# Kernel tuning notes

Measured on AMD Instinct MI355X. Metric: run time of the kernel, lower is better.

The kernel has to match this reference:

```python
import math
import jax, jax.numpy as jnp
import numpy as np

EMBED_DIM = 2048
NUM_HEADS = 16
HEAD_DIM = EMBED_DIM // NUM_HEADS
CHUNK = 128
RMS_EPS = 1e-5


def _build_slopes(n):
    # ALiBi-style slopes (power-of-2 branch; n=16 is a power of 2)
    def pow2(n):
        start = 2.0 ** (-(2.0 ** -(math.log2(n) - 3)))
        return [start * (start ** i) for i in range(n)]
    if math.log2(n).is_integer():
        s = pow2(n)
    else:
        closest = 2 ** math.floor(math.log2(n))
        s = pow2(closest) + pow2(2 * closest)[0::2][: n - closest]
    return jnp.asarray(s, dtype=jnp.float32)


def _rotary(x_BTHD, offset=0):
    # x: [B, T, H, D]; D//4 nonzero freqs + D//4 zero freqs -> D//2 angles
    T, D = x_BTHD.shape[1], x_BTHD.shape[-1]
    freq = (1.0 / 1024.0) ** jnp.linspace(0.0, 1.0, D // 4, dtype=jnp.float32)
    freq = jnp.concatenate([freq, jnp.zeros(D // 4, dtype=jnp.float32)])
    t = jnp.arange(offset, offset + T, dtype=jnp.float32)
    theta = t[:, None] * freq[None, :]            # [T, D/2]
    cos = jnp.cos(theta)[None, :, None, :]
    sin = jnp.sin(theta)[None, :, None, :]
    x1, x2 = jnp.split(x_BTHD.astype(jnp.float32), 2, axis=-1)
    y1 = x1 * cos + x2 * sin
    y2 = -x1 * sin + x2 * cos
    return jnp.concatenate([y1, y2], axis=-1).astype(x_BTHD.dtype)


def _lightning_attn(q, k, v, slopes):
    # q,k,v: [B, H, T, D]; decayed causal linear attention:
    #   o_t = q_t @ sum_{s<=t} exp(-slope*(t-s)) * k_s v_s^T
    B, H, T, D = q.shape
    C = CHUNK
    NC = T // C
    r = jnp.exp(-slopes)                          # [H]
    i = jnp.arange(C, dtype=jnp.float32)
    # factors within a chunk
    q_decay = r[:, None] ** (i[None, :] + 1.0)    # [H, C] : r^{i+1}
    k_decay = r[:, None] ** (C - 1.0 - i[None, :])  # [H, C] : r^{C-1-i}
    diff = i[:, None] - i[None, :]                # t - s
    mask = diff >= 0
    dmask = jnp.where(mask[None], r[:, None, None] ** jnp.where(mask, diff, 0.0)[None], 0.0)  # [H,C,C]
    r_C = r ** float(C)                            # [H]

    def reshape_chunks(x):
        return x.reshape(B, H, NC, C, D).transpose(2, 0, 1, 3, 4)  # [NC,B,H,C,D]

    qc, kc, vc = reshape_chunks(q), reshape_chunks(k), reshape_chunks(v)

    def step(kv, qkv):
        qi, ki, vi = qkv                          # [B,H,C,D]
        inter = jnp.einsum('bhcd,bhde->bhce', qi * q_decay[None, :, :, None], kv)
        scores = jnp.einsum('bhcd,bhsd->bhcs', qi, ki) * dmask[None]
        intra = jnp.einsum('bhcs,bhse->bhce', scores, vi)
        kv_new = r_C[None, :, None, None] * kv + jnp.einsum(
            'bhcd,bhce->bhde', ki * k_decay[None, :, :, None], vi)
        return kv_new, inter + intra

    kv0 = jnp.zeros((B, H, D, D), dtype=q.dtype)
    _, out = jax.lax.scan(step, kv0, (qc, kc, vc))  # [NC,B,H,C,D]
    return out.transpose(1, 2, 0, 3, 4).reshape(B, H, T, D)


def _rms_norm(x, w):
    var = jnp.mean(jnp.square(x), axis=-1, keepdims=True)
    return x * jax.lax.rsqrt(var + RMS_EPS) * w


def setup_inputs() -> dict:
    key = jax.random.key(0)
    ks = jax.random.split(key, 6)
    sc = 1.0 / math.sqrt(EMBED_DIM)
    return {
        'x': jax.random.normal(ks[0], (4, 4096, EMBED_DIM), dtype=jnp.float32),
        'Wq': jax.random.normal(ks[1], (EMBED_DIM, EMBED_DIM), dtype=jnp.float32) * sc,
        'Wk': jax.random.normal(ks[2], (EMBED_DIM, EMBED_DIM), dtype=jnp.float32) * sc,
        'Wv': jax.random.normal(ks[3], (EMBED_DIM, EMBED_DIM), dtype=jnp.float32) * sc,
        'Wo': jax.random.normal(ks[4], (EMBED_DIM, EMBED_DIM), dtype=jnp.float32) * sc,
        'rms_w': jnp.ones((EMBED_DIM,), dtype=jnp.float32),
    }


def reference(x, Wq, Wk, Wv, Wo, rms_w):
    B, T, E = x.shape
    H, D = NUM_HEADS, HEAD_DIM
    q = (x @ Wq).reshape(B, T, H, D)
    k = (x @ Wk).reshape(B, T, H, D)
    v = (x @ Wv).reshape(B, T, H, D)
    q = _rotary(q)
    k = _rotary(k)
    q, k, v = (t.transpose(0, 2, 1, 3) for t in (q, k, v))  # [B,H,T,D]
    slopes = _build_slopes(H)
    attn = _lightning_attn(q, k, v, slopes)       # [B,H,T,D]
    attn = attn.transpose(0, 2, 1, 3).reshape(B, T, E)
    attn = _rms_norm(attn, rms_w)
    return attn @ Wo
```

## Files before the change

### kernel.cpp

```cpp
#include <hip/hip_runtime.h>

typedef unsigned short ushort;
typedef float f32x4 __attribute__((ext_vector_type(4)));
typedef __bf16 bf16x8 __attribute__((ext_vector_type(8)));
typedef ushort u16x4 __attribute__((ext_vector_type(4)));
typedef ushort u16x8 __attribute__((ext_vector_type(8)));

#define LOG2E 1.4426950408889634f

__device__ __forceinline__ ushort f2bu(float f) { __bf16 b = (__bf16)f; return __builtin_bit_cast(ushort, b); }
__device__ __forceinline__ float  bu2f(ushort u) { return (float)__builtin_bit_cast(__bf16, u); }

__device__ __forceinline__ void gld16(const void* g, void* l) {
    __builtin_amdgcn_global_load_lds((const __attribute__((address_space(1))) unsigned int*)g,
                                     (__attribute__((address_space(3))) unsigned int*)l, 16, 0, 0);
}

__global__ __launch_bounds__(256) void k_cvt(const float* __restrict__ in, ushort* __restrict__ out, int n4) {
    int i = blockIdx.x * 256 + threadIdx.x;
    if (i < n4) {
        float4 v = ((const float4*)in)[i];
        u16x4 o = { f2bu(v.x), f2bu(v.y), f2bu(v.z), f2bu(v.w) };
        ((u16x4*)out)[i] = o;
    }
}

__global__ __launch_bounds__(256) void k_twt(const float* __restrict__ W, ushort* __restrict__ Wt) {
    __shared__ float t[32][33];
    int n0 = blockIdx.x * 32, k0 = blockIdx.y * 32;
    int tx = threadIdx.x & 31, ty = threadIdx.x >> 5;
#pragma unroll
    for (int i = 0; i < 32; i += 8) t[ty + i][tx] = W[(size_t)(k0 + ty + i) * 2048 + n0 + tx];
    __syncthreads();
#pragma unroll
    for (int i = 0; i < 32; i += 8) Wt[(size_t)(n0 + ty + i) * 2048 + k0 + tx] = f2bu(t[tx][ty + i]);
}

__global__ __launch_bounds__(256) void k_rope(float* __restrict__ tab) {
    int idx = blockIdx.x * 256 + threadIdx.x;
    int t = idx >> 5, j = idx & 31;
    float fr = exp2f(-10.0f * (float)j / 31.0f);
    float th = (float)t * fr;
    tab[idx * 2]     = cosf(th);
    tab[idx * 2 + 1] = sinf(th);
}

#define AOFF(buf, kh) ((buf) * 32768 + (kh) * 16384)
#define BOFF(buf, kh) (65536 + (buf) * 32768 + (kh) * 16384)

#define STG_A(BUFX, KHX, KKX) do {                                                 \
    gld16(asrc0 + ((KKX) + (KHX) * 32) * 2, lds + AOFF(BUFX, KHX) + ldst);         \
    gld16(asrc1 + ((KKX) + (KHX) * 32) * 2, lds + AOFF(BUFX, KHX) + 8192 + ldst);  \
} while (0)
#define STG_B(BUFX, KHX, KKX) do {                                                 \
    gld16(bsrc0 + ((KKX) + (KHX) * 32) * 2, lds + BOFF(BUFX, KHX) + ldst);         \
    gld16(bsrc1 + ((KKX) + (KHX) * 32) * 2, lds + BOFF(BUFX, KHX) + 8192 + ldst);  \
} while (0)

#define PHASE(BUF, KH, MH, LDB, STAGE_STMT, TAILVM) do {                           \
    bf16x8 af_[4];                                                                 \
    const char* ab_ = lds + AOFF(BUF, KH);                                         \
    _Pragma("unroll")                                                              \
    for (int mi_ = 0; mi_ < 4; ++mi_)                                              \
        af_[mi_] = *(const bf16x8*)(ab_ + offA[(MH) * 4 + mi_]);                   \
    if (LDB) {                                                                     \
        const char* bb_ = lds + BOFF(BUF, KH);                                     \
        _Pragma("unroll")                                                          \
        for (int ni_ = 0; ni_ < 4; ++ni_)                                          \
            bfr[ni_] = *(const bf16x8*)(bb_ + offB[ni_]);                          \
    }                                                                              \
    STAGE_STMT;                                                                    \
    __builtin_amdgcn_s_barrier();                                                  \
    asm volatile("s_waitcnt lgkmcnt(0)" ::: "memory");                             \
    __builtin_amdgcn_sched_barrier(0);                                             \
    __builtin_amdgcn_s_setprio(1);                                                 \
    _Pragma("unroll")                                                              \
    for (int mi_ = 0; mi_ < 4; ++mi_)                                              \
        _Pragma("unroll")                                                          \
        for (int ni_ = 0; ni_ < 4; ++ni_)                                          \
            acc[(MH) * 4 + mi_][ni_] = __builtin_amdgcn_mfma_f32_16x16x32_bf16(    \
                af_[mi_], bfr[ni_], acc[(MH) * 4 + mi_][ni_], 0, 0, 0);            \
    __builtin_amdgcn_s_setprio(0);                                                 \
    TAILVM;                                                                        \
    __builtin_amdgcn_s_barrier();                                                  \
} while (0)

#define TILE(BUF, TC) do {                                                         \
    int tp1_ = (TC) + 1 < 32 ? (TC) + 1 : 31;                                      \
    int tp2_ = (TC) + 2 < 32 ? (TC) + 2 : 31;                                      \
    int kb1_ = tp1_ * 64, kb2_ = tp2_ * 64;                                        \
    PHASE(BUF, 0, 0, 1, STG_A((BUF) ^ 1, 1, kb1_), ((void)0));                     \
    PHASE(BUF, 0, 1, 0, STG_B((BUF) ^ 1, 1, kb1_), ((void)0));                     \
    PHASE(BUF, 1, 0, 1, STG_A(BUF, 0, kb2_), ((void)0));                           \
    PHASE(BUF, 1, 1, 0, STG_B(BUF, 0, kb2_),                                       \
          asm volatile("s_waitcnt vmcnt(4)" ::: "memory"));                        \
} while (0)

template <int OUTF32>
__global__ __launch_bounds__(512, 2) void k_gemm(const ushort* __restrict__ A, const ushort* __restrict__ Bt,
                                                 float* __restrict__ Cf, ushort* __restrict__ Cb) {
    __shared__ __align__(128) char lds[131072];
    const int tid = threadIdx.x;
    const int wid = tid >> 6, lane = tid & 63;
    const int wm = wid >> 2, wn = wid & 3;
    const int lrow = lane & 15, q = lane >> 4;

    int bid = blockIdx.x;
    int xcd = bid & 7, local = bid >> 3;
    size_t m0 = (size_t)(xcd * 8 + (local >> 3)) * 256;
    size_t n0 = (size_t)(local & 7) * 256;

    int offA[8], offB[4];
#pragma unroll
    for (int mi = 0; mi < 8; ++mi) {
        int R = wm * 128 + mi * 16 + lrow;
        offA[mi] = R * 64 + ((q ^ ((R >> 1) & 3)) << 4);
    }
#pragma unroll
    for (int ni = 0; ni < 4; ++ni) {
        int R = wn * 64 + ni * 16 + lrow;
        offB[ni] = R * 64 + ((q ^ ((R >> 1) & 3)) << 4);
    }

    int srow0 = tid >> 2;
    int cw = (tid & 3) ^ ((tid >> 3) & 3);
    const char* asrc0 = (const char*)(A + (m0 + srow0) * 2048 + cw * 8);
    const char* asrc1 = (const char*)(A + (m0 + srow0 + 128) * 2048 + cw * 8);
    const char* bsrc0 = (const char*)(Bt + (n0 + srow0) * 2048 + cw * 8);
    const char* bsrc1 = (const char*)(Bt + (n0 + srow0 + 128) * 2048 + cw * 8);
    const int ldst = tid * 16;

    f32x4 acc[8][4] = {};
    bf16x8 bfr[4];

    STG_A(0, 0, 0); STG_B(0, 0, 0); STG_A(0, 1, 0); STG_B(0, 1, 0);
    STG_A(1, 0, 64); STG_B(1, 0, 64);
    asm volatile("s_waitcnt vmcnt(4)" ::: "memory");
    __builtin_amdgcn_s_barrier();

#pragma unroll 1
    for (int t = 0; t < 32; t += 2) {
        TILE(0, t);
        TILE(1, t + 1);
    }

#pragma unroll
    for (int mi = 0; mi < 8; ++mi)
#pragma unroll
        for (int ni = 0; ni < 4; ++ni)
#pragma unroll
            for (int i = 0; i < 4; ++i) {
                size_t row = m0 + wm * 128 + mi * 16 + (lane >> 4) * 4 + i;
                size_t col = n0 + wn * 64 + ni * 16 + lrow;
                if (OUTF32) Cf[row * 2048 + col] = acc[mi][ni][i];
                else        Cb[row * 2048 + col] = f2bu(acc[mi][ni][i]);
            }
}

__global__ __launch_bounds__(256) void k_reshape(const ushort* __restrict__ Cin, ushort* __restrict__ outN,
                                                 ushort* __restrict__ outT, const float* __restrict__ rt, int mode) {
    int blk = blockIdx.x;
    int c = blk & 31, bh = blk >> 5, b = bh >> 4, h = bh & 15;
    __shared__ __align__(16) ushort lt[128][136];
    int tid = threadIdx.x;
    int d = tid & 63, rq = tid >> 6;
    float slope = exp2f(-0.5f * (float)(h + 1));
    float l2r = -slope * LOG2E;
    for (int rp = 0; rp < 32; ++rp) {
        int tr = rp * 4 + rq;
        int t = c * 128 + tr;
        const ushort* src = Cin + ((size_t)(b * 4096 + t)) * 2048 + h * 128;
        float x1 = bu2f(src[d]), x2 = bu2f(src[d + 64]);
        float y1 = x1, y2 = x2;
        if (mode != 2 && d < 32) {
            float cs = rt[(t * 32 + d) * 2], sn = rt[(t * 32 + d) * 2 + 1];
            y1 = x1 * cs + x2 * sn;
            y2 = x2 * cs - x1 * sn;
        }
        if (mode != 2) {
            ushort* dstN = outN + ((size_t)bh * 4096 + t) * 128;
            dstN[d] = f2bu(y1); dstN[d + 64] = f2bu(y2);
        }
        if (mode != 0) { lt[tr][d] = f2bu(y1); lt[tr][d + 64] = f2bu(y2); }
    }
    if (mode == 0) return;
    __syncthreads();
    int dd = tid >> 1, half = tid & 1;
    ushort* dstT = outT + ((size_t)bh * 128 + dd) * 4096 + c * 128 + half * 64;
    for (int j8 = 0; j8 < 8; ++j8) {
        u16x8 tmp;
#pragma unroll
        for (int j = 0; j < 8; ++j) {
            int s = half * 64 + j8 * 8 + j;
            float v = bu2f(lt[s][dd]);
            if (mode == 1) v *= exp2f(l2r * (float)(127 - s));
            tmp[j] = f2bu(v);
        }
        *(u16x8*)(dstT + j8 * 8) = tmp;
    }
}

__global__ __launch_bounds__(256) void k_pass1(const ushort* __restrict__ kTa, const ushort* __restrict__ vTa,
                                               float* __restrict__ KVc) {
    int blk = blockIdx.x;
    int c = blk & 31, bh = blk >> 5;
    __shared__ __align__(16) ushort lv[128][136];
    __shared__ __align__(16) ushort lk[128][136];
    int tid = threadIdx.x;
#pragma unroll
    for (int i = 0; i < 8; ++i) {
        int idx = i * 256 + tid; int row = idx >> 4, cb = (idx & 15) * 8;
        *(bf16x8*)&lv[row][cb] = *(const bf16x8*)(vTa + ((size_t)bh * 128 + row) * 4096 + c * 128 + cb);
        *(bf16x8*)&lk[row][cb] = *(const bf16x8*)(kTa + ((size_t)bh * 128 + row) * 4096 + c * 128 + cb);
    }
    __syncthreads();
    int wid = tid >> 6, lane = tid & 63, wr = wid >> 1, wc = wid & 1;
    int lrow = lane & 15, lko = (lane >> 4) * 8;
    f32x4 acc[4][4] = {};
#pragma unroll
    for (int ks = 0; ks < 4; ++ks) {
        bf16x8 a[4], bb[4];
#pragma unroll
        for (int mi = 0; mi < 4; ++mi) a[mi] = *(const bf16x8*)&lv[wr * 64 + mi * 16 + lrow][ks * 32 + lko];
#pragma unroll
        for (int ni = 0; ni < 4; ++ni) bb[ni] = *(const bf16x8*)&lk[wc * 64 + ni * 16 + lrow][ks * 32 + lko];
#pragma unroll
        for (int mi = 0; mi < 4; ++mi)
#pragma unroll
            for (int ni = 0; ni < 4; ++ni)
                acc[mi][ni] = __builtin_amdgcn_mfma_f32_16x16x32_bf16(a[mi], bb[ni], acc[mi][ni], 0, 0, 0);
    }
    float* out = KVc + (size_t)blk * 16384;
#pragma unroll
    for (int mi = 0; mi < 4; ++mi)
#pragma unroll
        for (int ni = 0; ni < 4; ++ni)
#pragma unroll
            for (int i = 0; i < 4; ++i)
                out[(wr * 64 + mi * 16 + (lane >> 4) * 4 + i) * 128 + wc * 64 + ni * 16 + lrow] = acc[mi][ni][i];
}

__global__ __launch_bounds__(256) void k_scan(const float* __restrict__ KVc, ushort* __restrict__ KVbf) {
    int bh = blockIdx.x >> 4, seg = blockIdx.x & 15, h = bh & 15;
    float slope = exp2f(-0.5f * (float)(h + 1));
    float rC = exp2f(-slope * LOG2E * 128.0f);
    int off = seg * 1024 + threadIdx.x * 4;
    f32x4 st = {0.f, 0.f, 0.f, 0.f};
    for (int c = 0; c < 32; ++c) {
        size_t base = ((size_t)bh * 32 + c) * 16384 + off;
        f32x4 v = *(const f32x4*)(KVc + base);
        u16x4 o = { f2bu(st.x), f2bu(st.y), f2bu(st.z), f2bu(st.w) };
        *(u16x4*)(KVbf + base) = o;
        st = st * rC + v;
    }
}

__global__ __launch_bounds__(512) void k_pass3(const ushort* __restrict__ qa, const ushort* __restrict__ ka,
                                               const ushort* __restrict__ vTa, const ushort* __restrict__ KVbf,
                                               ushort* __restrict__ attn) {
    int blk = blockIdx.x;
    int c = blk & 31, bh = blk >> 5, h = bh & 15;
    __shared__ __align__(16) ushort lq[128][136];
    __shared__ __align__(16) ushort lk[128][136];
    __shared__ __align__(16) ushort lv[128][136];
    int tid = threadIdx.x;
#pragma unroll
    for (int i = 0; i < 4; ++i) {
        int idx = i * 512 + tid; int row = idx >> 4, cb = (idx & 15) * 8;
        *(bf16x8*)&lq[row][cb] = *(const bf16x8*)(qa + ((size_t)bh * 4096 + c * 128 + row) * 128 + cb);
        *(bf16x8*)&lk[row][cb] = *(const bf16x8*)(ka + ((size_t)bh * 4096 + c * 128 + row) * 128 + cb);
        *(bf16x8*)&lv[row][cb] = *(const bf16x8*)(vTa + ((size_t)bh * 128 + row) * 4096 + c * 128 + cb);
    }
    __syncthreads();
    int wid = tid >> 6, lane = tid & 63;
    int wr = wid >> 2, wc = wid & 3;
    int lrow = lane & 15, lko = (lane >> 4) * 8;
    float slope = exp2f(-0.5f * (float)(h + 1));
    float l2r = -slope * LOG2E;

    f32x4 accs[4][2] = {};
#pragma unroll
    for (int kd = 0; kd < 4; ++kd) {
        bf16x8 a[4], bb[2];
#pragma unroll
        for (int mi = 0; mi < 4; ++mi) a[mi] = *(const bf16x8*)&lq[wr * 64 + mi * 16 + lrow][kd * 32 + lko];
#pragma unroll
        for (int ni = 0; ni < 2; ++ni) bb[ni] = *(const bf16x8*)&lk[wc * 32 + ni * 16 + lrow][kd * 32 + lko];
#pragma unroll
        for (int mi = 0; mi < 4; ++mi)
#pragma unroll
            for (int ni = 0; ni < 2; ++ni)
                accs[mi][ni] = __builtin_amdgcn_mfma_f32_16x16x32_bf16(a[mi], bb[ni], accs[mi][ni], 0, 0, 0);
    }
    __syncthreads();

    f32x4 acc[4][2] = {};
#pragma unroll
    for (int kd = 0; kd < 4; ++kd) {
        bf16x8 a[4], bb[2];
#pragma unroll
        for (int mi = 0; mi < 4; ++mi) a[mi] = *(const bf16x8*)&lq[wr * 64 + mi * 16 + lrow][kd * 32 + lko];
#pragma unroll
        for (int ni = 0; ni < 2; ++ni)
            bb[ni] = *(const bf16x8*)(KVbf + (size_t)blk * 16384 + (size_t)(wc * 32 + ni * 16 + lrow) * 128 + kd * 32 + lko);
#pragma unroll
        for (int mi = 0; mi < 4; ++mi)
#pragma unroll
            for (int ni = 0; ni < 2; ++ni)
                acc[mi][ni] = __builtin_amdgcn_mfma_f32_16x16x32_bf16(a[mi], bb[ni], acc[mi][ni], 0, 0, 0);
    }

#pragma unroll
    for (int mi = 0; mi < 4; ++mi)
#pragma unroll
        for (int ni = 0; ni < 2; ++ni)
#pragma unroll
            for (int i = 0; i < 4; ++i) {
                int t = wr * 64 + mi * 16 + (lane >> 4) * 4 + i;
                int s = wc * 32 + ni * 16 + lrow;
                int dt = t - s;
                float w = (dt < 0) ? 0.f : exp2f(l2r * (float)dt);
                lk[t][s] = f2bu(accs[mi][ni][i] * w);
            }

#pragma unroll
    for (int mi = 0; mi < 4; ++mi)
#pragma unroll
        for (int ni = 0; ni < 2; ++ni)
#pragma unroll
            for (int i = 0; i < 4; ++i) {
                int t = wr * 64 + mi * 16 + (lane >> 4) * 4 + i;
                acc[mi][ni][i] *= exp2f(l2r * (float)(t + 1));
            }
    __syncthreads();

#pragma unroll
    for (int ks = 0; ks < 4; ++ks) {
        bf16x8 a[4], bb[2];
#pragma unroll
        for (int mi = 0; mi < 4; ++mi) a[mi] = *(const bf16x8*)&lk[wr * 64 + mi * 16 + lrow][ks * 32 + lko];
#pragma unroll
        for (int ni = 0; ni < 2; ++ni) bb[ni] = *(const bf16x8*)&lv[wc * 32 + ni * 16 + lrow][ks * 32 + lko];
#pragma unroll
        for (int mi = 0; mi < 4; ++mi)
#pragma unroll
            for (int ni = 0; ni < 2; ++ni)
                acc[mi][ni] = __builtin_amdgcn_mfma_f32_16x16x32_bf16(a[mi], bb[ni], acc[mi][ni], 0, 0, 0);
    }

    ushort* out = attn + ((size_t)bh * 4096 + c * 128) * 128;
#pragma unroll
    for (int mi = 0; mi < 4; ++mi)
#pragma unroll
        for (int ni = 0; ni < 2; ++ni)
#pragma unroll
            for (int i = 0; i < 4; ++i)
                out[(size_t)(wr * 64 + mi * 16 + (lane >> 4) * 4 + i) * 128 + wc * 32 + ni * 16 + lrow] =
                    f2bu(acc[mi][ni][i]);
}

__global__ __launch_bounds__(256) void k_rms(const ushort* __restrict__ attn, const float* __restrict__ w,
                                             ushort* __restrict__ normed) {
    int tok = blockIdx.x; int b = tok >> 12, t = tok & 4095;
    int tid = threadIdx.x;
    int e0 = tid * 8; int h = e0 >> 7, d0 = e0 & 127;
    bf16x8 v = *(const bf16x8*)(attn + (((size_t)(b * 16 + h) * 4096 + t) * 128 + d0));
    float f[8]; float ss = 0.f;
#pragma unroll
    for (int j = 0; j < 8; ++j) { f[j] = (float)v[j]; ss += f[j] * f[j]; }
#pragma unroll
    for (int o = 1; o < 64; o <<= 1) ss += __shfl_xor(ss, o, 64);
    __shared__ float red[4];
    if ((tid & 63) == 0) red[tid >> 6] = ss;
    __syncthreads();
    float tot = red[0] + red[1] + red[2] + red[3];
    float sc = rsqrtf(tot * (1.0f / 2048.0f) + 1e-5f);
    u16x8 ov;
#pragma unroll
    for (int j = 0; j < 8; ++j) ov[j] = f2bu(f[j] * sc * w[e0 + j]);
    *(u16x8*)(normed + (size_t)tok * 2048 + e0) = ov;
}

extern "C" void kernel_launch(void* const* d_in, const int* in_sizes, int n_in,
                              void* d_out, int out_size, void* d_ws, size_t ws_size,
                              hipStream_t stream) {
    const float* x    = (const float*)d_in[0];
    const float* Wq   = (const float*)d_in[1];
    const float* Wk   = (const float*)d_in[2];
    const float* Wv   = (const float*)d_in[3];
    const float* Wo   = (const float*)d_in[4];
    const float* rmsw = (const float*)d_in[5];
    char* ws = (char*)d_ws;
    const size_t MiB = 1ull << 20;
    ushort* WtQ  = (ushort*)(ws + 0);
    ushort* WtK  = (ushort*)(ws + 8 * MiB);
    ushort* WtV  = (ushort*)(ws + 16 * MiB);
    ushort* WtO  = (ushort*)(ws + 24 * MiB);
    ushort* xb   = (ushort*)(ws + 32 * MiB);
    ushort* Cbuf = (ushort*)(ws + 96 * MiB);
    ushort* qa   = (ushort*)(ws + 160 * MiB);
    ushort* ka   = (ushort*)(ws + 224 * MiB);
    ushort* kTa  = (ushort*)(ws + 288 * MiB);
    ushort* vTa  = (ushort*)(ws + 352 * MiB);
    float*  rt   = (float*)(ws + 416 * MiB);
    float*  KVc  = (float*)(ws + 32 * MiB);
    ushort* KVbf = (ushort*)(ws + 288 * MiB);
    ushort* attn = (ushort*)(ws + 32 * MiB);
    ushort* nrm  = (ushort*)(ws + 96 * MiB);

    k_cvt<<<32768, 256, 0, stream>>>(x, xb, 8388608);
    dim3 gw(64, 64);
    k_twt<<<gw, 256, 0, stream>>>(Wq, WtQ);
    k_twt<<<gw, 256, 0, stream>>>(Wk, WtK);
    k_twt<<<gw, 256, 0, stream>>>(Wv, WtV);
    k_twt<<<gw, 256, 0, stream>>>(Wo, WtO);
    k_rope<<<512, 256, 0, stream>>>(rt);

    k_gemm<0><<<512, 512, 0, stream>>>(xb, WtQ, nullptr, Cbuf);
    k_reshape<<<2048, 256, 0, stream>>>(Cbuf, qa, nullptr, rt, 0);
    k_gemm<0><<<512, 512, 0, stream>>>(xb, WtK, nullptr, Cbuf);
    k_reshape<<<2048, 256, 0, stream>>>(Cbuf, ka, kTa, rt, 1);
    k_gemm<0><<<512, 512, 0, stream>>>(xb, WtV, nullptr, Cbuf);
    k_reshape<<<2048, 256, 0, stream>>>(Cbuf, nullptr, vTa, rt, 2);

    k_pass1<<<2048, 256, 0, stream>>>(kTa, vTa, KVc);
    k_scan<<<1024, 256, 0, stream>>>(KVc, KVbf);
    k_pass3<<<2048, 512, 0, stream>>>(qa, ka, vTa, KVbf, attn);

    k_rms<<<16384, 256, 0, stream>>>(attn, rmsw, nrm);
    k_gemm<1><<<512, 512, 0, stream>>>(nrm, WtO, (float*)d_out, nullptr);
}
```

Before: 898.0 us.

## Fuse Q/K/V projections into one GEMM launch with XCD column-stripe mapping

The three projection GEMMs are replaced by a single 1536-block launch over the concatenated transposed weights, which are already contiguous in the workspace. Each output column tile is routed to its own Q, K or V buffer, and the workspace is re-laid out so all three results coexist before the reshape kernels. The block-to-tile mapping now gives each XCD a fixed stripe of N tiles across all M, aiming for better weight reuse in L2. The global-load wait counts are also relaxed, with an extra wait added mid-tile, which changes how load and compute overlap in the GEMM pipeline.

```diff
diff --git a/kernel.cpp b/kernel.cpp
--- a/kernel.cpp
+++ b/kernel.cpp
@@ -90,15 +90,17 @@
     int tp2_ = (TC) + 2 < 32 ? (TC) + 2 : 31;                                      \
     int kb1_ = tp1_ * 64, kb2_ = tp2_ * 64;                                        \
     PHASE(BUF, 0, 0, 1, STG_A((BUF) ^ 1, 1, kb1_), ((void)0));                     \
-    PHASE(BUF, 0, 1, 0, STG_B((BUF) ^ 1, 1, kb1_), ((void)0));                     \
+    PHASE(BUF, 0, 1, 0, STG_B((BUF) ^ 1, 1, kb1_),                                 \
+          asm volatile("s_waitcnt vmcnt(8)" ::: "memory"));                        \
     PHASE(BUF, 1, 0, 1, STG_A(BUF, 0, kb2_), ((void)0));                           \
     PHASE(BUF, 1, 1, 0, STG_B(BUF, 0, kb2_),                                       \
-          asm volatile("s_waitcnt vmcnt(4)" ::: "memory"));                        \
+          asm volatile("s_waitcnt vmcnt(8)" ::: "memory"));                        \
 } while (0)
 
-template <int OUTF32>
+template <int OUTF32, int NPX>
 __global__ __launch_bounds__(512, 2) void k_gemm(const ushort* __restrict__ A, const ushort* __restrict__ Bt,
-                                                 float* __restrict__ Cf, ushort* __restrict__ Cb) {
+                                                 float* __restrict__ Cf, ushort* __restrict__ C0,
+                                                 ushort* __restrict__ C1, ushort* __restrict__ C2) {
     __shared__ __align__(128) char lds[131072];
     const int tid = threadIdx.x;
     const int wid = tid >> 6, lane = tid & 63;
@@ -107,8 +109,9 @@
 
     int bid = blockIdx.x;
     int xcd = bid & 7, local = bid >> 3;
-    size_t m0 = (size_t)(xcd * 8 + (local >> 3)) * 256;
-    size_t n0 = (size_t)(local & 7) * 256;
+    int nloc = local % NPX, mloc = local / NPX;
+    size_t n0 = (size_t)(xcd * NPX + nloc) * 256;
+    size_t m0 = (size_t)mloc * 256;
 
     int offA[8], offB[4];
 #pragma unroll
@@ -135,7 +138,7 @@
 
     STG_A(0, 0, 0); STG_B(0, 0, 0); STG_A(0, 1, 0); STG_B(0, 1, 0);
     STG_A(1, 0, 64); STG_B(1, 0, 64);
-    asm volatile("s_waitcnt vmcnt(4)" ::: "memory");
+    asm volatile("s_waitcnt vmcnt(8)" ::: "memory");
     __builtin_amdgcn_s_barrier();
 
 #pragma unroll 1
@@ -144,6 +147,9 @@
         TILE(1, t + 1);
     }
 
+    int tsel = (int)(n0 >> 11);
+    size_t ncol = n0 & 2047;
+    ushort* Cb = (tsel == 0) ? C0 : ((tsel == 1) ? C1 : C2);
 #pragma unroll
     for (int mi = 0; mi < 8; ++mi)
 #pragma unroll
@@ -151,9 +157,9 @@
 #pragma unroll
             for (int i = 0; i < 4; ++i) {
                 size_t row = m0 + wm * 128 + mi * 16 + (lane >> 4) * 4 + i;
-                size_t col = n0 + wn * 64 + ni * 16 + lrow;
-                if (OUTF32) Cf[row * 2048 + col] = acc[mi][ni][i];
-                else        Cb[row * 2048 + col] = f2bu(acc[mi][ni][i]);
+                size_t col = wn * 64 + ni * 16 + lrow;
+                if (OUTF32) Cf[row * 2048 + n0 + col] = acc[mi][ni][i];
+                else        Cb[row * 2048 + ncol + col] = f2bu(acc[mi][ni][i]);
             }
 }
 
@@ -392,41 +398,41 @@
     const float* rmsw = (const float*)d_in[5];
     char* ws = (char*)d_ws;
     const size_t MiB = 1ull << 20;
-    ushort* WtQ  = (ushort*)(ws + 0);
-    ushort* WtK  = (ushort*)(ws + 8 * MiB);
-    ushort* WtV  = (ushort*)(ws + 16 * MiB);
-    ushort* WtO  = (ushort*)(ws + 24 * MiB);
-    ushort* xb   = (ushort*)(ws + 32 * MiB);
-    ushort* Cbuf = (ushort*)(ws + 96 * MiB);
-    ushort* qa   = (ushort*)(ws + 160 * MiB);
-    ushort* ka   = (ushort*)(ws + 224 * MiB);
-    ushort* kTa  = (ushort*)(ws + 288 * MiB);
-    ushort* vTa  = (ushort*)(ws + 352 * MiB);
-    float*  rt   = (float*)(ws + 416 * MiB);
-    float*  KVc  = (float*)(ws + 32 * MiB);
-    ushort* KVbf = (ushort*)(ws + 288 * MiB);
-    ushort* attn = (ushort*)(ws + 32 * MiB);
-    ushort* nrm  = (ushort*)(ws + 96 * MiB);
+    ushort* WtQKV = (ushort*)(ws + 0);
+    ushort* WtK   = (ushort*)(ws + 8 * MiB);
+    ushort* WtV   = (ushort*)(ws + 16 * MiB);
+    ushort* WtO   = (ushort*)(ws + 24 * MiB);
+    ushort* xb    = (ushort*)(ws + 32 * MiB);
+    ushort* CQ    = (ushort*)(ws + 96 * MiB);
+    ushort* CK    = (ushort*)(ws + 160 * MiB);
+    ushort* CV    = (ushort*)(ws + 224 * MiB);
+    ushort* qa    = (ushort*)(ws + 288 * MiB);
+    ushort* ka    = (ushort*)(ws + 352 * MiB);
+    float*  rt    = (float*)(ws + 416 * MiB);
+    ushort* kTa   = (ushort*)(ws + 32 * MiB);
+    ushort* vTa   = (ushort*)(ws + 96 * MiB);
+    float*  KVc   = (float*)(ws + 160 * MiB);
+    ushort* KVbf  = (ushort*)(ws + 32 * MiB);
+    ushort* attn  = (ushort*)(ws + 224 * MiB);
+    ushort* nrm   = (ushort*)(ws + 96 * MiB);
 
     k_cvt<<<32768, 256, 0, stream>>>(x, xb, 8388608);
     dim3 gw(64, 64);
-    k_twt<<<gw, 256, 0, stream>>>(Wq, WtQ);
+    k_twt<<<gw, 256, 0, stream>>>(Wq, WtQKV);
     k_twt<<<gw, 256, 0, stream>>>(Wk, WtK);
     k_twt<<<gw, 256, 0, stream>>>(Wv, WtV);
     k_twt<<<gw, 256, 0, stream>>>(Wo, WtO);
     k_rope<<<512, 256, 0, stream>>>(rt);
 
-    k_gemm<0><<<512, 512, 0, stream>>>(xb, WtQ, nullptr, Cbuf);
-    k_reshape<<<2048, 256, 0, stream>>>(Cbuf, qa, nullptr, rt, 0);
-    k_gemm<0><<<512, 512, 0, stream>>>(xb, WtK, nullptr, Cbuf);
-    k_reshape<<<2048, 256, 0, stream>>>(Cbuf, ka, kTa, rt, 1);
-    k_gemm<0><<<512, 512, 0, stream>>>(xb, WtV, nullptr, Cbuf);
-    k_reshape<<<2048, 256, 0, stream>>>(Cbuf, nullptr, vTa, rt, 2);
+    k_gemm<0, 3><<<1536, 512, 0, stream>>>(xb, WtQKV, nullptr, CQ, CK, CV);
+    k_reshape<<<2048, 256, 0, stream>>>(CQ, qa, nullptr, rt, 0);
+    k_reshape<<<2048, 256, 0, stream>>>(CK, ka, kTa, rt, 1);
+    k_reshape<<<2048, 256, 0, stream>>>(CV, nullptr, vTa, rt, 2);
 
     k_pass1<<<2048, 256, 0, stream>>>(kTa, vTa, KVc);
     k_scan<<<1024, 256, 0, stream>>>(KVc, KVbf);
     k_pass3<<<2048, 512, 0, stream>>>(qa, ka, vTa, KVbf, attn);
 
     k_rms<<<16384, 256, 0, stream>>>(attn, rmsw, nrm);
-    k_gemm<1><<<512, 512, 0, stream>>>(nrm, WtO, (float*)d_out, nullptr);
-}
+    k_gemm<1, 1><<<512, 512, 0, stream>>>(nrm, WtO, (float*)d_out, nullptr, nullptr, nullptr);
+}
```

Result: slower. 994.9 us (+10.8%).
